# Kernel optimization log

Measured on AMD Instinct MI355X. Metric: run time of the kernel, lower is better.

The kernel has to match this reference:

```python
import jax, jax.numpy as jnp
from jax import lax
import numpy as np

LATENT = 512
LABEL = 128
BATCH = 1024


def _maxpool2(x):
    # 2x2 max pool, stride 2, NCHW
    return lax.reduce_window(x, -jnp.inf, lax.max, (1, 1, 2, 2), (1, 1, 2, 2), 'VALID')


def _encoder(x, c1w, c1b, c2w, c2b, fw, fb):
    dn = ('NCHW', 'OIHW', 'NCHW')
    y = lax.conv_general_dilated(x, c1w, (1, 1), 'SAME', dimension_numbers=dn)
    y = _maxpool2(jax.nn.relu(y + c1b[None, :, None, None]))  # [B,32,14,14]
    y = lax.conv_general_dilated(y, c2w, (1, 1), 'SAME', dimension_numbers=dn)
    y = _maxpool2(jax.nn.relu(y + c2b[None, :, None, None]))  # [B,64,7,7]
    y = y.reshape(y.shape[0], -1)                              # [B,3136]
    return y @ fw.T + fb                                       # [B,latent]


def _hopfield_w(rep):
    # rho = mean over ALL elements (matches torch.mean(x))
    rho = jnp.mean(rep)
    t = rep - rho                      # [label, latent]
    w = t.T @ t                        # sum of rank-1 outer products
    w = w * (1.0 - jnp.eye(w.shape[0], dtype=w.dtype))  # zero diagonal
    return w / LABEL


def _clustering(lat, w):
    # batched fixed-length Hopfield relaxation with min-energy tracking
    s0 = jnp.tanh(lat)                 # [B,L]
    B = s0.shape[0]

    def step(carry, _):
        s, min_e, min_s = carry
        prev = lax.stop_gradient(s)    # torch detaches prev_s each iter
        s_new = jnp.abs(prev) * jnp.sign(prev @ w.T)      # [B,L]
        e = -jnp.einsum('bi,ij,bj->b', s_new, w, s_new)    # [B]
        better = e < min_e
        min_e = jnp.where(better, e, min_e)
        min_s = jnp.where(better[:, None], s_new, min_s)
        return (s_new, min_e, min_s), None

    init = (s0, jnp.full((B,), jnp.inf, dtype=s0.dtype), jnp.zeros_like(s0))
    (_, _, min_s), _ = lax.scan(step, init, None, length=LATENT)
    return min_s


def setup_inputs() -> dict:
    key = jax.random.key(0)
    ks = jax.random.split(key, 11)
    d = {}
    d['image'] = jax.random.normal(ks[0], (BATCH, 1, 28, 28), dtype=jnp.float32)
    d['label_images'] = jax.random.uniform(ks[1], (LABEL, 1, 28, 28), dtype=jnp.float32)
    d['conv1_w'] = jax.random.normal(ks[2], (32, 1, 5, 5), dtype=jnp.float32) * 0.1
    d['conv1_b'] = jnp.zeros((32,), dtype=jnp.float32)
    d['conv2_w'] = jax.random.normal(ks[3], (64, 32, 5, 5), dtype=jnp.float32) * 0.05
    d['conv2_b'] = jnp.zeros((64,), dtype=jnp.float32)
    d['fc1_w'] = jax.random.normal(ks[4], (LATENT, 64 * 7 * 7), dtype=jnp.float32) * 0.02
    d['fc1_b'] = jnp.zeros((LATENT,), dtype=jnp.float32)
    d['fcn_w'] = jax.random.normal(ks[5], (LABEL, LATENT), dtype=jnp.float32) * 0.05
    d['fcn_b'] = jnp.zeros((LABEL,), dtype=jnp.float32)
    return d


def reference(image, label_images, conv1_w, conv1_b, conv2_w, conv2_b,
              fc1_w, fc1_b, fcn_w, fcn_b):
    rep = jnp.tanh(_encoder(label_images, conv1_w, conv1_b, conv2_w, conv2_b, fc1_w, fc1_b))  # [label,L]
    lat = _encoder(image, conv1_w, conv1_b, conv2_w, conv2_b, fc1_w, fc1_b)                    # [B,L]
    # FCN on detached latents (torch: .clone().detach())
    label = jax.nn.softmax(lax.stop_gradient(lat) @ fcn_w.T + fcn_b, axis=1)                   # [B,label]
    w = _hopfield_w(rep)                                                                        # [L,L]
    min_s = _clustering(lat, w)                                                                 # [B,L]
    out = jax.nn.softmax(jnp.abs(min_s @ rep.T), axis=1)                                        # [B,label]
    return (out, label)
```

## Files before the change

### kernel.cpp

```cpp
#include <hip/hip_runtime.h>
#include <hip/hip_bf16.h>
#include <math.h>

#define BATCH 1024
#define LABEL 128
#define LATENT 512
#define NTOT 1152

typedef short short8 __attribute__((ext_vector_type(8)));
typedef float f32x16 __attribute__((ext_vector_type(16)));

__device__ __forceinline__ unsigned short f2bf(float f) {
    __hip_bfloat16 h = __float2bfloat16(f);
    return *(unsigned short*)&h;
}
__device__ __forceinline__ float bf2f(unsigned short u) {
    __hip_bfloat16 h; *(unsigned short*)&h = u;
    return __bfloat162float(h);
}


__global__ __launch_bounds__(256) void conv1_pool(const float* __restrict__ image,
                                                  const float* __restrict__ limg,
                                                  const float* __restrict__ wt,
                                                  const float* __restrict__ bias,
                                                  unsigned short* __restrict__ o1b) {
    const int n = blockIdx.x;
    const float* in = (n < BATCH) ? (image + (size_t)n * 784)
                                  : (limg + (size_t)(n - BATCH) * 784);
    __shared__ float pin[32][32];
    __shared__ float wts[32 * 25];
    const int tid = threadIdx.x;
    unsigned short* ob = o1b + (size_t)n * 12800;
    for (int i = tid; i < 256; i += 256) {
        int pl_ = i >> 7, r = i & 127;
        ob[pl_ * 6400 + 6272 + r] = 0;
    }
    for (int idx = tid; idx < 32 * 32; idx += 256) ((float*)pin)[idx] = 0.f;
    __syncthreads();
    for (int idx = tid; idx < 784; idx += 256) {
        int y = idx / 28, x = idx % 28;
        pin[y + 2][x + 2] = in[idx];
    }
    for (int idx = tid; idx < 800; idx += 256) wts[idx] = wt[idx];
    __syncthreads();
    const int oc = tid & 31;
    float wk[25];
    #pragma unroll
    for (int k = 0; k < 25; ++k) wk[k] = wts[oc * 25 + k];
    float b = bias[oc];
    const int slot_lo = (oc & 7);
    const int gq = oc >> 3;
    for (int o = tid; o < 6272; o += 256) {
        int p = o >> 5, py = p / 14, px = p % 14;
        float win[6][6];
        #pragma unroll
        for (int r = 0; r < 6; ++r)
        #pragma unroll
        for (int c = 0; c < 6; ++c)
            win[r][c] = pin[2 * py + r][2 * px + c];
        float a00 = b, a01 = b, a10 = b, a11 = b;
        #pragma unroll
        for (int ky = 0; ky < 5; ++ky)
        #pragma unroll
        for (int kx = 0; kx < 5; ++kx) {
            float w = wk[ky * 5 + kx];
            a00 = fmaf(win[ky][kx], w, a00);
            a01 = fmaf(win[ky][kx + 1], w, a01);
            a10 = fmaf(win[ky + 1][kx], w, a10);
            a11 = fmaf(win[ky + 1][kx + 1], w, a11);
        }
        float v = fmaxf(fmaxf(fmaxf(a00, a01), fmaxf(a10, a11)), 0.f);
        unsigned short b1 = f2bf(v); float r1 = v - bf2f(b1);
        unsigned short b2 = f2bf(r1);
        int off = p * 32 + (((gq ^ (p >> 1)) & 3) << 3) + slot_lo;
        ob[off] = b1; ob[6400 + off] = b2;
    }
}

__global__ __launch_bounds__(256) void bprep(const float* __restrict__ w,
                                             unsigned short* __restrict__ Bf) {
    int idx = blockIdx.x * 256 + threadIdx.x;
    if (idx >= 102400) return;
    int j = idx & 7, lane = (idx >> 3) & 63, ocT = (idx >> 9) & 1, s = idx >> 10;
    int q = lane >> 5, nn = lane & 31;
    int k = 16 * s + 8 * q + j;
    int tap = k >> 5, ic = k & 31;
    int oc = 32 * ocT + nn;
    float v = w[oc * 800 + ic * 25 + tap];
    unsigned short b1 = f2bf(v);
    unsigned short b2 = f2bf(v - bf2f(b1));
    size_t base = ((size_t)(s * 2 + ocT) * 2) * 512 + lane * 8 + j;
    Bf[base] = b1; Bf[base + 512] = b2;
}

#define BSTR ((size_t)512 * 3136)
#define ASTR ((size_t)NTOT * 3136)
__global__ __launch_bounds__(256) void wprep(const float* __restrict__ w,
                                             unsigned short* __restrict__ B3) {
    int idx = blockIdx.x * 256 + threadIdx.x;
    if (idx >= 512 * 3136) return;
    float v = w[idx];
    unsigned short b1 = f2bf(v);
    float r1 = v - bf2f(b1);
    unsigned short b2 = f2bf(r1);
    unsigned short b3 = f2bf(r1 - bf2f(b2));
    B3[idx] = b1; B3[BSTR + idx] = b2; B3[2 * BSTR + idx] = b3;
}

__global__ __launch_bounds__(256) void conv2_mfma(const unsigned short* __restrict__ o1b,
                                                  const unsigned short* __restrict__ Bf,
                                                  const float* __restrict__ bias,
                                                  unsigned short* __restrict__ out3) {
    const int n = blockIdx.x;
    __shared__ __align__(16) unsigned short pl[12800];
    const int tid = threadIdx.x;
    const int lane = tid & 63, wv = tid >> 6;
    const int ocT = wv & 1, kh = wv >> 1;

    {
        const float4* src = (const float4*)(o1b + (size_t)n * 12800);
        float4* dst = (float4*)pl;
        for (int i = tid; i < 1600; i += 256) dst[i] = src[i];
    }
    __syncthreads();

    const int m_ = lane & 31, q = lane >> 5;
    int ym[7], xm[7], mm[7];
    #pragma unroll
    for (int t = 0; t < 7; ++t) {
        int m = 32 * t + m_;
        mm[t] = m;
        ym[t] = m / 14;
        xm[t] = m - 14 * ym[t];
    }
    f32x16 acc[7];
    {
        float bs = (kh == 0) ? bias[32 * ocT + m_] : 0.f;
        #pragma unroll
        for (int t = 0; t < 7; ++t)
        #pragma unroll
        for (int r = 0; r < 16; ++r) acc[t][r] = bs;
    }

    for (int s = kh * 25; s < kh * 25 + 25; ++s) {
        const unsigned short* bp = Bf + ((size_t)(s * 2 + ocT) * 2) * 512 + lane * 8;
        short8 b1 = *(const short8*)(bp);
        short8 b2 = *(const short8*)(bp + 512);
        int kb = 16 * s + 8 * q;
        int tap = kb >> 5, ic0 = kb & 31, g = ic0 >> 3;
        int ky = (tap * 13) >> 6;
        int kx = tap - ky * 5;
        int iyk = ky - 2, ixk = kx - 2;
        int pq2 = iyk * 14 + ixk;
        short8 a1[7], a2[7];
        #pragma unroll
        for (int t = 0; t < 7; ++t) {
            int iy = ym[t] + iyk, ix = xm[t] + ixk;
            int valid = ((unsigned)iy < 14u) & ((unsigned)ix < 14u);
            int cpt = valid ? (mm[t] + pq2) : 196;
            int addr = cpt * 32 + (((g ^ (cpt >> 1)) & 3) << 3);
            a1[t] = *(const short8*)(pl + addr);
            a2[t] = *(const short8*)(pl + 6400 + addr);
        }
        #pragma unroll
        for (int t = 0; t < 7; ++t)
            acc[t] = __builtin_amdgcn_mfma_f32_32x32x16_bf16(a1[t], b1, acc[t], 0, 0, 0);
        #pragma unroll
        for (int t = 0; t < 7; ++t)
            acc[t] = __builtin_amdgcn_mfma_f32_32x32x16_bf16(a1[t], b2, acc[t], 0, 0, 0);
        #pragma unroll
        for (int t = 0; t < 7; ++t)
            acc[t] = __builtin_amdgcn_mfma_f32_32x32x16_bf16(a2[t], b1, acc[t], 0, 0, 0);
    }
    __syncthreads();

    float* accbuf = (float*)pl;
    #pragma unroll
    for (int ph = 0; ph < 3; ++ph) {
        const int t0 = 3 * ph;
        const int tn = (ph == 2) ? 1 : 3;
        if (kh == 0) {
            for (int t = t0; t < t0 + tn; ++t)
                #pragma unroll
                for (int r = 0; r < 16; ++r)
                    accbuf[((ocT * tn + (t - t0)) * 16 + r) * 64 + lane] = acc[t][r];
        }
        __syncthreads();
        if (kh == 1) {
            for (int t = t0; t < t0 + tn; ++t)
                #pragma unroll
                for (int r = 0; r < 16; ++r)
                    acc[t][r] += accbuf[((ocT * tn + (t - t0)) * 16 + r) * 64 + lane];
        }
        __syncthreads();
    }

    float* hx = (float*)pl;
    if (kh == 1) {
        const int oc = 32 * ocT + m_;
        #pragma unroll
        for (int t = 0; t < 7; ++t)
        #pragma unroll
        for (int e = 0; e < 8; ++e) {
            const int reg = 2 * e;
            const int r = (reg & 3) + 8 * (reg >> 2) + 4 * q;
            const int m = 32 * t + r;
            if (m < 196) {
                float xm2 = fmaxf(acc[t][reg], acc[t][reg + 1]);
                int y = (m * 2341) >> 15;
                int px = (m - 14 * y) >> 1;
                hx[(y * 7 + px) * 65 + oc] = xm2;
            }
        }
    }
    __syncthreads();

    const size_t OSTR = ASTR;
    for (int idx = tid; idx < 3136; idx += 256) {
        int oc2 = (idx * 2675) >> 17;
        int p = idx - 49 * oc2;
        int py = (p * 9363) >> 16;
        int px = p - 7 * py;
        float v = fmaxf(hx[(2 * py * 7 + px) * 65 + oc2],
                        hx[((2 * py + 1) * 7 + px) * 65 + oc2]);
        v = fmaxf(v, 0.f);
        unsigned short b1 = f2bf(v);
        float r1 = v - bf2f(b1);
        unsigned short b2 = f2bf(r1);
        unsigned short b3 = f2bf(r1 - bf2f(b2));
        size_t o = (size_t)n * 3136 + idx;
        out3[o] = b1; out3[OSTR + o] = b2; out3[2 * OSTR + o] = b3;
    }
}

__global__ __launch_bounds__(256) void fc1_mfma(const unsigned short* __restrict__ A3,
                                                const unsigned short* __restrict__ B3,
                                                float* __restrict__ part) {
    __shared__ unsigned short As[3][2048];
    __shared__ unsigned short Bs[3][2048];
    const int tid = threadIdx.x;
    const int n0 = blockIdx.x * 64, m0 = blockIdx.y * 64;
    const int koff = blockIdx.z * 448;
    const int lr = tid >> 2, g = tid & 3;
    const int slot = (((g ^ (lr >> 1)) & 3) << 3);
    const int lane = tid & 63, wv = tid >> 6;
    const int nq = wv & 1, mq = wv >> 1;
    const int q = lane >> 5, l31 = lane & 31;
    const int rA = 32 * nq + l31, rB = 32 * mq + l31;
    f32x16 acc;
    #pragma unroll
    for (int r = 0; r < 16; ++r) acc[r] = 0.f;

    for (int bk = 0; bk < 448; bk += 32) {
        const size_t ka = (size_t)(koff + bk + (g << 3));
        short8 av[3], bv[3];
        #pragma unroll
        for (int p = 0; p < 3; ++p) {
            av[p] = *(const short8*)(A3 + p * ASTR + (size_t)(n0 + lr) * 3136 + ka);
            bv[p] = *(const short8*)(B3 + p * BSTR + (size_t)(m0 + lr) * 3136 + ka);
        }
        __syncthreads();
        #pragma unroll
        for (int p = 0; p < 3; ++p) {
            *(short8*)&As[p][(lr << 5) + slot] = av[p];
            *(short8*)&Bs[p][(lr << 5) + slot] = bv[p];
        }
        __syncthreads();
        #pragma unroll
        for (int s2 = 0; s2 < 32; s2 += 16) {
            const int gg = (s2 + (q << 3)) >> 3;
            const int sa = (((gg ^ (rA >> 1)) & 3) << 3);
            const int sb = (((gg ^ (rB >> 1)) & 3) << 3);
            short8 a1 = *(const short8*)&As[0][(rA << 5) + sa];
            short8 a2 = *(const short8*)&As[1][(rA << 5) + sa];
            short8 a3 = *(const short8*)&As[2][(rA << 5) + sa];
            short8 b1 = *(const short8*)&Bs[0][(rB << 5) + sb];
            short8 b2 = *(const short8*)&Bs[1][(rB << 5) + sb];
            short8 b3 = *(const short8*)&Bs[2][(rB << 5) + sb];
            acc = __builtin_amdgcn_mfma_f32_32x32x16_bf16(a1, b1, acc, 0, 0, 0);
            acc = __builtin_amdgcn_mfma_f32_32x32x16_bf16(a1, b2, acc, 0, 0, 0);
            acc = __builtin_amdgcn_mfma_f32_32x32x16_bf16(a2, b1, acc, 0, 0, 0);
            acc = __builtin_amdgcn_mfma_f32_32x32x16_bf16(a2, b2, acc, 0, 0, 0);
            acc = __builtin_amdgcn_mfma_f32_32x32x16_bf16(a1, b3, acc, 0, 0, 0);
            acc = __builtin_amdgcn_mfma_f32_32x32x16_bf16(a3, b1, acc, 0, 0, 0);
        }
    }
    float* pb = part + (size_t)blockIdx.z * NTOT * 512;
    #pragma unroll
    for (int reg = 0; reg < 16; ++reg) {
        int nn = n0 + 32 * nq + (reg & 3) + 8 * (reg >> 2) + 4 * q;
        int mmo = m0 + 32 * mq + l31;
        pb[(size_t)nn * 512 + mmo] = acc[reg];
    }
}

__global__ __launch_bounds__(256) void fc1_reduce(const float* __restrict__ part,
                                                  const float* __restrict__ bias,
                                                  float* __restrict__ lat,
                                                  float* __restrict__ rep) {
    int idx = blockIdx.x * 256 + threadIdx.x;
    int m = idx & 511;
    float v = bias[m];
    #pragma unroll
    for (int kz = 0; kz < 7; ++kz) v += part[(size_t)kz * NTOT * 512 + idx];
    if (idx < BATCH * 512) lat[idx] = v;
    else rep[idx - BATCH * 512] = tanhf(v);
}

__global__ __launch_bounds__(128) void fcn_softmax(const float* __restrict__ lat,
                                                   const float* __restrict__ fw,
                                                   const float* __restrict__ fb,
                                                   float* __restrict__ out) {
    const int b = blockIdx.x;
    const int j = threadIdx.x;
    __shared__ float lrow[512];
    __shared__ float red[128];
    for (int i = j; i < 512; i += 128) lrow[i] = lat[b * 512 + i];
    __syncthreads();
    const float4* w4 = (const float4*)(fw + j * 512);
    float acc = fb[j];
    #pragma unroll 4
    for (int qq = 0; qq < 128; ++qq) {
        float4 a = ((const float4*)lrow)[qq];
        float4 w = w4[qq];
        acc += a.x * w.x + a.y * w.y + a.z * w.z + a.w * w.w;
    }
    red[j] = acc;
    __syncthreads();
    for (int off = 64; off >= 1; off >>= 1) {
        if (j < off) red[j] = fmaxf(red[j], red[j + off]);
        __syncthreads();
    }
    float mx = red[0];
    __syncthreads();
    float ex = expf(acc - mx);
    red[j] = ex;
    __syncthreads();
    for (int off = 64; off >= 1; off >>= 1) {
        if (j < off) red[j] += red[j + off];
        __syncthreads();
    }
    out[b * 128 + j] = ex / red[0];
}

__global__ __launch_bounds__(256) void rho_kernel(const float* __restrict__ rep,
                                                  float* __restrict__ rho) {
    __shared__ float red[256];
    const int tid = threadIdx.x;
    float s = 0.f;
    for (int i = tid; i < LABEL * LATENT; i += 256) s += rep[i];
    red[tid] = s;
    __syncthreads();
    for (int off = 128; off >= 1; off >>= 1) {
        if (tid < off) red[tid] += red[tid + off];
        __syncthreads();
    }
    if (tid == 0) rho[0] = red[0] / (float)(LABEL * LATENT);
}

__global__ __launch_bounds__(256) void t_kernel(const float* __restrict__ rep,
                                                const float* __restrict__ rho,
                                                float* __restrict__ tT) {
    int idx = blockIdx.x * 256 + threadIdx.x;
    int i = idx / 128, k = idx % 128;
    tT[idx] = rep[k * 512 + i] - rho[0];
}

__global__ __launch_bounds__(256) void w_kernel(const float* __restrict__ tT,
                                                float* __restrict__ w) {
    int idx = blockIdx.x * 256 + threadIdx.x;
    int i = idx >> 9, j = idx & 511;
    const float4* a = (const float4*)(tT + i * 128);
    const float4* b = (const float4*)(tT + j * 128);
    float acc = 0.f;
    #pragma unroll 8
    for (int q = 0; q < 32; ++q) {
        float4 av = a[q], bv = b[q];
        acc += av.x * bv.x + av.y * bv.y + av.z * bv.z + av.w * bv.w;
    }
    w[idx] = (i == j) ? 0.f : acc * (1.f / 128.f);
}

#define CB 4
__device__ __forceinline__ float sgnf(float x) {
    return (x > 0.f) ? 1.f : ((x < 0.f) ? -1.f : 0.f);
}

__global__ __launch_bounds__(256) void clustering(const float* __restrict__ lat,
                                                  const float* __restrict__ w,
                                                  const float* __restrict__ rep,
                                                  float* __restrict__ out) {
    const int tid = threadIdx.x;
    const int row0 = blockIdx.x * CB;
    __shared__ float sbuf[CB][512];
    __shared__ float mins[CB][512];
    __shared__ float red[256];
    __shared__ float part_e[4][CB];
    __shared__ int part_c[4];
    __shared__ float min_e[CB];
    __shared__ int copyf[CB];
    __shared__ int donef[CB];
    __shared__ int cnt[CB];
    __shared__ int jidx[CB][512];
    __shared__ float jdel[CB][512];
    const int i0 = 2 * tid, i1 = 2 * tid + 1;
    const int wave = tid >> 6, lane = tid & 63;

    float sm10[CB], sm11[CB], sm20[CB], sm21[CB], h0[CB], h1[CB];
    #pragma unroll
    for (int r = 0; r < CB; ++r) {
        float a = tanhf(lat[(row0 + r) * 512 + i0]);
        float b = tanhf(lat[(row0 + r) * 512 + i1]);
        sm10[r] = a; sm11[r] = b;
        sm20[r] = a; sm21[r] = b;
        sbuf[r][i0] = a; sbuf[r][i1] = b;
        h0[r] = 0.f; h1[r] = 0.f;
    }
    if (tid < CB) { min_e[tid] = INFINITY; donef[tid] = 0; cnt[tid] = 0; }
    __syncthreads();

    #pragma unroll 4
    for (int j = 0; j < 512; ++j) {
        float2 wvv = *(const float2*)(w + (size_t)j * 512 + i0);
        #pragma unroll
        for (int r = 0; r < CB; ++r) {
            float sj = sbuf[r][j];
            h0[r] = fmaf(sj, wvv.x, h0[r]);
            h1[r] = fmaf(sj, wvv.y, h1[r]);
        }
    }

    for (int k = 1; k <= 512; ++k) {
        float sn0[CB], sn1[CB];
        int cy = 0xF;
        #pragma unroll
        for (int r = 0; r < CB; ++r) {
            int dn = donef[r];
            if (dn) {
                sn0[r] = sm10[r]; sn1[r] = sm11[r];
            } else {
                sn0[r] = fabsf(sm10[r]) * sgnf(h0[r]);
                sn1[r] = fabsf(sm11[r]) * sgnf(h1[r]);
                if (!(sn0[r] == sm20[r] && sn1[r] == sm21[r])) cy &= ~(1 << r);
                if (sn0[r] != sm10[r]) {
                    int p = atomicAdd(&cnt[r], 1);
                    jidx[r][p] = i0; jdel[r][p] = sn0[r] - sm10[r];
                }
                if (sn1[r] != sm11[r]) {
                    int p = atomicAdd(&cnt[r], 1);
                    jidx[r][p] = i1; jdel[r][p] = sn1[r] - sm11[r];
                }
            }
        }
        #pragma unroll
        for (int m = 32; m >= 1; m >>= 1) cy &= __shfl_xor(cy, m, 64);
        if (lane == 0) part_c[wave] = cy;
        __syncthreads();

        #pragma unroll
        for (int r = 0; r < CB; ++r) {
            const int c = cnt[r];
            for (int t = 0; t < c; ++t) {
                const int j = jidx[r][t];
                const float d = jdel[r][t];
                const float2 wvv = *(const float2*)(w + (size_t)j * 512 + i0);
                h0[r] = fmaf(d, wvv.x, h0[r]);
                h1[r] = fmaf(d, wvv.y, h1[r]);
            }
        }
        float ep[CB];
        #pragma unroll
        for (int r = 0; r < CB; ++r) ep[r] = sn0[r] * h0[r] + sn1[r] * h1[r];
        #pragma unroll
        for (int m = 32; m >= 1; m >>= 1) {
            #pragma unroll
            for (int r = 0; r < CB; ++r) ep[r] += __shfl_xor(ep[r], m, 64);
        }
        if (lane == 0) {
            #pragma unroll
            for (int r = 0; r < CB; ++r) part_e[wave][r] = ep[r];
        }
        __syncthreads();

        if (tid < CB) {
            int r = tid;
            if (!donef[r]) {
                float e = -(part_e[0][r] + part_e[1][r] + part_e[2][r] + part_e[3][r]);
                int better = e < min_e[r];
                if (better) min_e[r] = e;
                copyf[r] = better;
                int fl = part_c[0] & part_c[1] & part_c[2] & part_c[3];
                int fixedp = (cnt[r] == 0);
                int cyc = (k >= 2) && ((fl >> r) & 1);
                if (fixedp || cyc) donef[r] = 1;
            } else {
                copyf[r] = 0;
            }
            cnt[r] = 0;
        }
        __syncthreads();

        int alldone = 1;
        #pragma unroll
        for (int r = 0; r < CB; ++r) {
            if (copyf[r]) { mins[r][i0] = sn0[r]; mins[r][i1] = sn1[r]; }
            alldone &= donef[r];
            sm20[r] = sm10[r]; sm21[r] = sm11[r];
            sm10[r] = sn0[r];  sm11[r] = sn1[r];
        }
        if (alldone) break;
    }
    __syncthreads();

    const int j = tid & 127, half = tid >> 7;
    for (int r = 0; r < CB; ++r) {
        const float4* rr = (const float4*)(rep + (size_t)j * 512 + half * 256);
        const float4* ms = (const float4*)(&mins[r][half * 256]);
        float p = 0.f;
        #pragma unroll 8
        for (int q = 0; q < 64; ++q) {
            float4 rv = rr[q], mv = ms[q];
            p += rv.x * mv.x + rv.y * mv.y + rv.z * mv.z + rv.w * mv.w;
        }
        red[tid] = p;
        __syncthreads();
        float v = 0.f;
        if (tid < 128) { v = fabsf(red[tid] + red[tid + 128]); red[tid] = v; }
        __syncthreads();
        for (int off = 64; off >= 1; off >>= 1) {
            if (tid < off) red[tid] = fmaxf(red[tid], red[tid + off]);
            __syncthreads();
        }
        float mx = red[0];
        __syncthreads();
        float ex = 0.f;
        if (tid < 128) { ex = expf(v - mx); red[tid] = ex; }
        __syncthreads();
        for (int off = 64; off >= 1; off >>= 1) {
            if (tid < off) red[tid] += red[tid + off];
            __syncthreads();
        }
        if (tid < 128) out[(size_t)(row0 + r) * 128 + tid] = ex / red[0];
        __syncthreads();
    }
}

extern "C" void kernel_launch(void* const* d_in, const int* in_sizes, int n_in,
                              void* d_out, int out_size, void* d_ws, size_t ws_size,
                              hipStream_t stream) {
    const float* image = (const float*)d_in[0];
    const float* limg  = (const float*)d_in[1];
    const float* c1w   = (const float*)d_in[2];
    const float* c1b   = (const float*)d_in[3];
    const float* c2w   = (const float*)d_in[4];
    const float* c2b   = (const float*)d_in[5];
    const float* f1w   = (const float*)d_in[6];
    const float* f1b   = (const float*)d_in[7];
    const float* fnw   = (const float*)d_in[8];
    const float* fnb   = (const float*)d_in[9];
    float* out = (float*)d_out;
    float* ws  = (float*)d_ws;

    unsigned short* o1b  = (unsigned short*)ws;
    unsigned short* out3 = o1b + (size_t)NTOT * 12800;
    float* lat  = (float*)(out3 + 3 * ASTR);
    float* rep  = lat + (size_t)BATCH * 512;
    float* tT   = rep + (size_t)LABEL * 512;
    float* wmat = tT + (size_t)512 * 128;
    float* rho  = wmat + (size_t)512 * 512;
    unsigned short* Bw3   = (unsigned short*)(rho + 16);
    unsigned short* Bfrag = Bw3 + 3 * BSTR;
    float* part = (float*)ws;

    hipLaunchKernelGGL(bprep, dim3(400), dim3(256), 0, stream, c2w, Bfrag);
    hipLaunchKernelGGL(wprep, dim3(6272), dim3(256), 0, stream, f1w, Bw3);
    hipLaunchKernelGGL(conv1_pool, dim3(NTOT), dim3(256), 0, stream, image, limg, c1w, c1b, o1b);
    hipLaunchKernelGGL(conv2_mfma, dim3(NTOT), dim3(256), 0, stream, o1b, Bfrag, c2b, out3);
    hipLaunchKernelGGL(fc1_mfma, dim3(NTOT / 64, 512 / 64, 7), dim3(256), 0, stream,
                       out3, Bw3, part);
    hipLaunchKernelGGL(fc1_reduce, dim3(NTOT * 512 / 256), dim3(256), 0, stream,
                       part, f1b, lat, rep);
    hipLaunchKernelGGL(fcn_softmax, dim3(BATCH), dim3(128), 0, stream, lat, fnw, fnb,
                       out + (size_t)BATCH * LABEL);
    hipLaunchKernelGGL(rho_kernel, dim3(1), dim3(256), 0, stream, rep, rho);
    hipLaunchKernelGGL(t_kernel, dim3(256), dim3(256), 0, stream, rep, rho, tT);
    hipLaunchKernelGGL(w_kernel, dim3(1024), dim3(256), 0, stream, tT, wmat);
    hipLaunchKernelGGL(clustering, dim3(BATCH / CB), dim3(256), 0, stream, lat, wmat, rep, out);
}
```

Measured before the change: 446.7 us.

## Split conv2 waves over output rows and halve clustering rows per block

The conv2 MFMA kernel now splits the four waves by output-position tiles (mh) instead of by K halves (kh). This removes the shared-memory cross-wave accumulator reduction and its barriers, but each wave now loops over all 50 K steps, and the upper half wastes one of four tiles. The clustering kernel drops from 4 to 2 rows per block, doubling the number of blocks for more parallelism at the cost of more W reads per row. It also adds unroll pragmas on the h init and delta-update loops.

After: 426.2 us. 1.05x faster.

```diff
diff --git a/kernel.cpp b/kernel.cpp
--- a/kernel.cpp
+++ b/kernel.cpp
@@ -116,7 +116,7 @@
     __shared__ __align__(16) unsigned short pl[12800];
     const int tid = threadIdx.x;
     const int lane = tid & 63, wv = tid >> 6;
-    const int ocT = wv & 1, kh = wv >> 1;
+    const int ocT = wv & 1, mh = wv >> 1;
 
     {
         const float4* src = (const float4*)(o1b + (size_t)n * 12800);
@@ -126,24 +126,26 @@
     __syncthreads();
 
     const int m_ = lane & 31, q = lane >> 5;
-    int ym[7], xm[7], mm[7];
+    int ym[4], xm[4], mm[4], tvv[4];
     #pragma unroll
-    for (int t = 0; t < 7; ++t) {
+    for (int tt = 0; tt < 4; ++tt) {
+        int t = 4 * mh + tt;
+        tvv[tt] = (t < 7);
         int m = 32 * t + m_;
-        mm[t] = m;
-        ym[t] = m / 14;
-        xm[t] = m - 14 * ym[t];
-    }
-    f32x16 acc[7];
+        mm[tt] = m;
+        ym[tt] = m / 14;
+        xm[tt] = m - 14 * ym[tt];
+    }
+    f32x16 acc[4];
     {
-        float bs = (kh == 0) ? bias[32 * ocT + m_] : 0.f;
-        #pragma unroll
-        for (int t = 0; t < 7; ++t)
-        #pragma unroll
-        for (int r = 0; r < 16; ++r) acc[t][r] = bs;
-    }
-
-    for (int s = kh * 25; s < kh * 25 + 25; ++s) {
+        float bs = bias[32 * ocT + m_];
+        #pragma unroll
+        for (int tt = 0; tt < 4; ++tt)
+        #pragma unroll
+        for (int r = 0; r < 16; ++r) acc[tt][r] = bs;
+    }
+
+    for (int s = 0; s < 50; ++s) {
         const unsigned short* bp = Bf + ((size_t)(s * 2 + ocT) * 2) * 512 + lane * 8;
         short8 b1 = *(const short8*)(bp);
         short8 b2 = *(const short8*)(bp + 512);
@@ -153,61 +155,40 @@
         int kx = tap - ky * 5;
         int iyk = ky - 2, ixk = kx - 2;
         int pq2 = iyk * 14 + ixk;
-        short8 a1[7], a2[7];
-        #pragma unroll
-        for (int t = 0; t < 7; ++t) {
-            int iy = ym[t] + iyk, ix = xm[t] + ixk;
-            int valid = ((unsigned)iy < 14u) & ((unsigned)ix < 14u);
-            int cpt = valid ? (mm[t] + pq2) : 196;
+        short8 a1[4], a2[4];
+        #pragma unroll
+        for (int tt = 0; tt < 4; ++tt) {
+            int iy = ym[tt] + iyk, ix = xm[tt] + ixk;
+            int valid = tvv[tt] & ((unsigned)iy < 14u) & ((unsigned)ix < 14u);
+            int cpt = valid ? (mm[tt] + pq2) : 196;
             int addr = cpt * 32 + (((g ^ (cpt >> 1)) & 3) << 3);
-            a1[t] = *(const short8*)(pl + addr);
-            a2[t] = *(const short8*)(pl + 6400 + addr);
-        }
-        #pragma unroll
-        for (int t = 0; t < 7; ++t)
-            acc[t] = __builtin_amdgcn_mfma_f32_32x32x16_bf16(a1[t], b1, acc[t], 0, 0, 0);
-        #pragma unroll
-        for (int t = 0; t < 7; ++t)
-            acc[t] = __builtin_amdgcn_mfma_f32_32x32x16_bf16(a1[t], b2, acc[t], 0, 0, 0);
-        #pragma unroll
-        for (int t = 0; t < 7; ++t)
-            acc[t] = __builtin_amdgcn_mfma_f32_32x32x16_bf16(a2[t], b1, acc[t], 0, 0, 0);
-    }
-    __syncthreads();
-
-    float* accbuf = (float*)pl;
-    #pragma unroll
-    for (int ph = 0; ph < 3; ++ph) {
-        const int t0 = 3 * ph;
-        const int tn = (ph == 2) ? 1 : 3;
-        if (kh == 0) {
-            for (int t = t0; t < t0 + tn; ++t)
-                #pragma unroll
-                for (int r = 0; r < 16; ++r)
-                    accbuf[((ocT * tn + (t - t0)) * 16 + r) * 64 + lane] = acc[t][r];
-        }
-        __syncthreads();
-        if (kh == 1) {
-            for (int t = t0; t < t0 + tn; ++t)
-                #pragma unroll
-                for (int r = 0; r < 16; ++r)
-                    acc[t][r] += accbuf[((ocT * tn + (t - t0)) * 16 + r) * 64 + lane];
-        }
-        __syncthreads();
-    }
+            a1[tt] = *(const short8*)(pl + addr);
+            a2[tt] = *(const short8*)(pl + 6400 + addr);
+        }
+        #pragma unroll
+        for (int tt = 0; tt < 4; ++tt)
+            acc[tt] = __builtin_amdgcn_mfma_f32_32x32x16_bf16(a1[tt], b1, acc[tt], 0, 0, 0);
+        #pragma unroll
+        for (int tt = 0; tt < 4; ++tt)
+            acc[tt] = __builtin_amdgcn_mfma_f32_32x32x16_bf16(a1[tt], b2, acc[tt], 0, 0, 0);
+        #pragma unroll
+        for (int tt = 0; tt < 4; ++tt)
+            acc[tt] = __builtin_amdgcn_mfma_f32_32x32x16_bf16(a2[tt], b1, acc[tt], 0, 0, 0);
+    }
+    __syncthreads();
 
     float* hx = (float*)pl;
-    if (kh == 1) {
+    {
         const int oc = 32 * ocT + m_;
         #pragma unroll
-        for (int t = 0; t < 7; ++t)
+        for (int tt = 0; tt < 4; ++tt)
         #pragma unroll
         for (int e = 0; e < 8; ++e) {
             const int reg = 2 * e;
             const int r = (reg & 3) + 8 * (reg >> 2) + 4 * q;
-            const int m = 32 * t + r;
+            const int m = 32 * (4 * mh + tt) + r;
             if (m < 196) {
-                float xm2 = fmaxf(acc[t][reg], acc[t][reg + 1]);
+                float xm2 = fmaxf(acc[tt][reg], acc[tt][reg + 1]);
                 int y = (m * 2341) >> 15;
                 int px = (m - 14 * y) >> 1;
                 hx[(y * 7 + px) * 65 + oc] = xm2;
@@ -382,7 +363,7 @@
     w[idx] = (i == j) ? 0.f : acc * (1.f / 128.f);
 }
 
-#define CB 4
+#define CB 2
 __device__ __forceinline__ float sgnf(float x) {
     return (x > 0.f) ? 1.f : ((x < 0.f) ? -1.f : 0.f);
 }
@@ -420,7 +401,7 @@
     if (tid < CB) { min_e[tid] = INFINITY; donef[tid] = 0; cnt[tid] = 0; }
     __syncthreads();
 
-    #pragma unroll 4
+    #pragma unroll 8
     for (int j = 0; j < 512; ++j) {
         float2 wvv = *(const float2*)(w + (size_t)j * 512 + i0);
         #pragma unroll
@@ -433,7 +414,7 @@
 
     for (int k = 1; k <= 512; ++k) {
         float sn0[CB], sn1[CB];
-        int cy = 0xF;
+        int cy = (1 << CB) - 1;
         #pragma unroll
         for (int r = 0; r < CB; ++r) {
             int dn = donef[r];
@@ -461,6 +442,7 @@
         #pragma unroll
         for (int r = 0; r < CB; ++r) {
             const int c = cnt[r];
+            #pragma unroll 4
             for (int t = 0; t < c; ++t) {
                 const int j = jidx[r][t];
                 const float d = jdel[r][t];
```
